# Performance work log

Hardware: AMD Instinct MI355X
Metric: run time of the kernel (lower is better)

## Reference

```python
import jax, jax.numpy as jnp
import numpy as np

LEAKY_SLOPE = 0.01  # torch nn.LeakyReLU default


def leaky_relu(x):
    return jnp.where(x >= 0, x, LEAKY_SLOPE * x)


def rgcn_conv(x, edge_index, edge_type, w_rel, w_root, b_conv):
    # PyG RGCNConv: out = x @ W_root + b + sum_r mean_{edges of rel r into i}(x_src @ W_r)
    n = x.shape[0]
    src, dst = edge_index[0], edge_index[1]
    out = x @ w_root + b_conv
    num_rel = w_rel.shape[0]
    for r in range(num_rel):  # small fixed relation count
        mask = (edge_type == r)
        msg = x[src] @ w_rel[r]                      # [E, H]
        msg = jnp.where(mask[:, None], msg, 0.0)
        agg = jax.ops.segment_sum(msg, dst, num_segments=n)          # [N, H]
        cnt = jax.ops.segment_sum(mask.astype(x.dtype), dst, num_segments=n)
        out = out + agg / jnp.maximum(cnt, 1.0)[:, None]             # mean aggr
    return out


def setup_inputs() -> dict:
    key = jax.random.key(0)
    ks = jax.random.split(key, 10)
    N, E, D_IN, H, OUT, R = 50000, 600000, 768, 128, 3, 2
    s_in = 1.0 / np.sqrt(D_IN)
    s_h = 1.0 / np.sqrt(H)
    return {
        "feature": jax.random.normal(ks[0], (N, D_IN), dtype=jnp.float32),
        "edge_index": jax.random.randint(ks[1], (2, E), 0, N, dtype=jnp.int64),
        "edge_type": jax.random.randint(ks[2], (E,), 0, R, dtype=jnp.int64),
        "w_in": jax.random.uniform(ks[3], (D_IN, H), jnp.float32, -s_in, s_in),
        "b_in": jax.random.uniform(ks[4], (H,), jnp.float32, -s_in, s_in),
        "w_rel": jax.random.uniform(ks[5], (R, H, H), jnp.float32, -s_h, s_h),
        "w_root": jax.random.uniform(ks[6], (H, H), jnp.float32, -s_h, s_h),
        "b_conv": jnp.zeros((H,), jnp.float32),
        "w_out": jax.random.uniform(ks[7], (H, OUT), jnp.float32, -s_h, s_h),
        "b_out": jax.random.uniform(ks[8], (OUT,), jnp.float32, -s_h, s_h),
    }


def reference(feature, edge_index, edge_type, w_in, b_in, w_rel, w_root, b_conv, w_out, b_out):
    x = leaky_relu(feature @ w_in + b_in)
    # NOTE: original forward applies rgcn1 twice (shared weights); dropout is
    # identity at inference; rgcn2/linear_relu_output1 are unused.
    x = rgcn_conv(x, edge_index, edge_type, w_rel, w_root, b_conv)
    x = rgcn_conv(x, edge_index, edge_type, w_rel, w_root, b_conv)
    return x @ w_out + b_out
```

## Files before the change

### kernel.cpp

```cpp
#include <hip/hip_runtime.h>

#define H 128
#define CAP 64

typedef _Float16 f16x8 __attribute__((ext_vector_type(8)));
typedef float    f32x4 __attribute__((ext_vector_type(4)));

__global__ __launch_bounds__(256) void hist_fill(const int* __restrict__ src,
    const int* __restrict__ dst, const int* __restrict__ et,
    int* __restrict__ cnt, int* __restrict__ elist, int E, int N)
{
    int e = blockIdx.x * 256 + threadIdx.x;
    if (e >= E) return;
    int s = src[e], d = dst[e], t = et[e];
    int b = t * N + d;
    int pos = atomicAdd(&cnt[b], 1);
    if (pos < CAP) elist[(size_t)b * CAP + pos] = s;
}

__global__ __launch_bounds__(256) void prep_w(const float* __restrict__ w_in,
    const float* __restrict__ w_root, const float* __restrict__ w_rel,
    _Float16* __restrict__ wInT, _Float16* __restrict__ wcatT, int K)
{
    int idx = blockIdx.x * 256 + threadIdx.x;
    int tot1 = K * H;
    if (idx < tot1) {
        int k = idx >> 7, c = idx & 127;
        int o = ((k >> 3) << 10) + (c << 3) + (k & 7);
        wInT[o] = (_Float16)w_in[idx];
    } else {
        int i2 = idx - tot1;
        if (i2 < H * 384) {
            int c = i2 / 384, k = i2 - c * 384;
            float v;
            if (k < 128)      v = w_root[(size_t)k * H + c];
            else if (k < 256) v = w_rel[(size_t)(k - 128) * H + c];
            else              v = w_rel[(size_t)H * H + (size_t)(k - 256) * H + c];
            wcatT[i2] = (_Float16)v;
        }
    }
}

__global__ __launch_bounds__(256) void prep_fin(const float* __restrict__ w_root,
    const float* __restrict__ w_rel, const float* __restrict__ b_conv,
    const float* __restrict__ w_out, const float* __restrict__ b_out,
    float* __restrict__ wfin, float* __restrict__ bfin, int OUT)
{
    int idx = blockIdx.x * 256 + threadIdx.x;
    int nw = 3 * H * OUT;
    if (idx < nw) {
        int mk = idx / OUT, c = idx - mk * OUT;
        int m = mk >> 7, k = mk & 127;
        const float* W = (m == 0) ? w_root : (w_rel + (size_t)(m - 1) * H * H);
        float s = 0.f;
        for (int j = 0; j < H; j++)
            s += W[(size_t)k * H + j] * w_out[(size_t)j * OUT + c];
        wfin[(size_t)mk * OUT + c] = s;
    } else if (idx < nw + OUT) {
        int c = idx - nw;
        float s = b_out[c];
        for (int j = 0; j < H; j++) s += b_conv[j] * w_out[(size_t)j * OUT + c];
        bfin[c] = s;
    }
}

__device__ __forceinline__ f16x8 cvt8(float4 v0, float4 v1) {
    f16x8 t;
    t[0] = (_Float16)v0.x; t[1] = (_Float16)v0.y; t[2] = (_Float16)v0.z; t[3] = (_Float16)v0.w;
    t[4] = (_Float16)v1.x; t[5] = (_Float16)v1.y; t[6] = (_Float16)v1.z; t[7] = (_Float16)v1.w;
    return t;
}

__global__ __launch_bounds__(256, 2) void gemm_big(const float* __restrict__ A,
    const _Float16* __restrict__ WP, const float* __restrict__ bias,
    _Float16* __restrict__ C16, int M, int K, int ldc)
{
    __shared__ float As[2][4][2048];

    const int tid = threadIdx.x;
    const int w   = tid >> 6;
    const int l   = tid & 63;
    const int l15 = l & 15;
    const int q   = l >> 4;
    const int brow = blockIdx.x * 64;
    const int wr   = w * 16;

    const int lh  = l >> 5;
    const int l31 = l & 31;

    const _Float16* bp = WP + ((size_t)q * H + l15) * 8;

    float bj[8];
#pragma unroll
    for (int j = 0; j < 8; j++) bj[j] = bias[j * 16 + l15];

    f32x4 acc[8];
    const f32x4 z4 = {0.f, 0.f, 0.f, 0.f};
#pragma unroll
    for (int j = 0; j < 8; j++) acc[j] = z4;

    const int chunks = K / 128;

#define STAGE(c, nbuf)                                                          \
    {                                                                           \
        _Pragma("unroll")                                                       \
        for (int i = 0; i < 8; i++) {                                           \
            int r  = 2 * i + lh;                                                \
            int gr = brow + wr + r; if (gr >= M) gr = M - 1;                    \
            int cg = l31 ^ (r & 7);                                             \
            const float* ga = A + (size_t)gr * K + (c) * 128 + cg * 4;          \
            __builtin_amdgcn_global_load_lds(                                   \
                (const __attribute__((address_space(1))) void*)ga,              \
                (__attribute__((address_space(3))) void*)&As[nbuf][w][i * 256], \
                16, 0, 0);                                                      \
        }                                                                       \
    }

    STAGE(0, 0);
    __syncthreads();

    for (int c = 0; c < chunks; c++) {
        if (c + 1 < chunks) STAGE(c + 1, (c + 1) & 1);

        const float* wbuf = As[c & 1][w];
#pragma unroll
        for (int ks = 0; ks < 4; ks++) {
            const int sl = ks * 4 + q;
            const int xr = l15 & 7;
            const int p0 = (2 * sl) ^ xr;
            const int p1 = (2 * sl + 1) ^ xr;
            float4 lo = *(const float4*)&wbuf[l15 * 128 + p0 * 4];
            float4 hi = *(const float4*)&wbuf[l15 * 128 + p1 * 4];
            f16x8 af = cvt8(lo, hi);
            const _Float16* bks = bp + (size_t)(c * 4 + ks) * 4096;
            f16x8 bf[8];
#pragma unroll
            for (int j = 0; j < 8; j++) bf[j] = *(const f16x8*)(bks + j * 128);
#pragma unroll
            for (int j = 0; j < 8; j++)
                acc[j] = __builtin_amdgcn_mfma_f32_16x16x32_f16(af, bf[j], acc[j], 0, 0, 0);
        }
        __syncthreads();
    }
#undef STAGE

#pragma unroll
    for (int rg = 0; rg < 4; rg++) {
        int row = brow + wr + q * 4 + rg;
        if (row < M) {
#pragma unroll
            for (int j = 0; j < 8; j++) {
                float v = acc[j][rg] + bj[j];
                v = (v >= 0.f) ? v : 0.01f * v;
                C16[(size_t)row * ldc + j * 16 + l15] = (_Float16)v;
            }
        }
    }
}

template<int MODE>
__global__ __launch_bounds__(256) void gather_k(const _Float16* __restrict__ X,
    int ldx, _Float16* __restrict__ Mout, const int* __restrict__ elist,
    const int* __restrict__ cnt, int N,
    const float* __restrict__ wfin, const float* __restrict__ bfin,
    float* __restrict__ out)
{
    int wv = blockIdx.x * 4 + (threadIdx.x >> 6);
    int l  = threadIdx.x & 63;
    if (wv >= N) return;

    const int eo   = l >> 4;
    const int e2   = eo & 1;
    const int half = l >> 5;
    const int c8   = (l & 15) * 8;

    int dr = cnt[(size_t)half * N + wv];
    int d  = dr < CAP ? dr : CAP;
    float inv = dr > 0 ? 1.f / (float)dr : 0.f;
    const int* lst = elist + ((size_t)half * N + wv) * CAP;

    float acc[8];
#pragma unroll
    for (int j = 0; j < 8; j++) acc[j] = 0.f;

    const f16x8 zv = {};
    for (int p = e2; p < d; p += 8) {
        int p1 = p + 2, p2 = p + 4, p3 = p + 6;
        int s0 = lst[p];
        f16x8 v0 = *(const f16x8*)&X[(size_t)s0 * ldx + c8];
        f16x8 v1 = zv, v2 = zv, v3 = zv;
        if (p1 < d) { int s = lst[p1]; v1 = *(const f16x8*)&X[(size_t)s * ldx + c8]; }
        if (p2 < d) { int s = lst[p2]; v2 = *(const f16x8*)&X[(size_t)s * ldx + c8]; }
        if (p3 < d) { int s = lst[p3]; v3 = *(const f16x8*)&X[(size_t)s * ldx + c8]; }
#pragma unroll
        for (int j = 0; j < 8; j++)
            acc[j] += (float)v0[j] + (float)v1[j] + (float)v2[j] + (float)v3[j];
    }

#pragma unroll
    for (int j = 0; j < 8; j++) {
        acc[j] += __shfl_xor(acc[j], 16);
        acc[j] *= inv;
    }

    if (MODE == 0) {
        if (eo == 0 || eo == 2) {
            f16x8 o;
#pragma unroll
            for (int j = 0; j < 8; j++) o[j] = (_Float16)acc[j];
            *(f16x8*)&Mout[(size_t)wv * 256 + half * 128 + c8] = o;
        }
    } else {
        float p0 = 0.f, p1 = 0.f, p2 = 0.f;
        if (eo == 1) {
            f16x8 xv = *(const f16x8*)&X[(size_t)wv * ldx + c8];
#pragma unroll
            for (int j = 0; j < 8; j++) {
                float xf = (float)xv[j];
                const float* wr = wfin + (size_t)(c8 + j) * 3;
                p0 += xf * wr[0]; p1 += xf * wr[1]; p2 += xf * wr[2];
            }
        } else if (eo == 0 || eo == 2) {
            const float* wb = wfin + (size_t)(eo == 0 ? 1 : 2) * H * 3;
#pragma unroll
            for (int j = 0; j < 8; j++) {
                const float* wr = wb + (size_t)(c8 + j) * 3;
                p0 += acc[j] * wr[0]; p1 += acc[j] * wr[1]; p2 += acc[j] * wr[2];
            }
        }
#pragma unroll
        for (int off = 1; off <= 32; off <<= 1) {
            p0 += __shfl_xor(p0, off);
            p1 += __shfl_xor(p1, off);
            p2 += __shfl_xor(p2, off);
        }
        if (l == 0) {
            out[(size_t)wv * 3 + 0] = p0 + bfin[0];
            out[(size_t)wv * 3 + 1] = p1 + bfin[1];
            out[(size_t)wv * 3 + 2] = p2 + bfin[2];
        }
    }
}

__global__ __launch_bounds__(512) void gemm_cat(const _Float16* __restrict__ X1,
    const _Float16* __restrict__ Mt, const _Float16* __restrict__ WT,
    const float* __restrict__ bias, _Float16* __restrict__ X2, int M, int mtiles)
{
    const int w   = threadIdx.x >> 6;
    const int l   = threadIdx.x & 63;
    const int l15 = l & 15;
    const int q   = l >> 4;
    const int col = w * 16 + l15;

    f16x8 bf[12];
    {
        const _Float16* wpp = WT + (size_t)col * 384 + q * 8;
#pragma unroll
        for (int c = 0; c < 12; c++) bf[c] = *(const f16x8*)(wpp + c * 32);
    }
    const float bj = bias[col];

    int t = blockIdx.x;
    if (t >= mtiles) return;
    f16x8 xf[12];
    {
        const _Float16* xp = X1 + ((size_t)t * 16 + l15) * 128 + q * 8;
        const _Float16* mp = Mt + ((size_t)t * 16 + l15) * 256 + q * 8;
#pragma unroll
        for (int c = 0; c < 4; c++) xf[c] = *(const f16x8*)(xp + c * 32);
#pragma unroll
        for (int c = 4; c < 12; c++) xf[c] = *(const f16x8*)(mp + (c - 4) * 32);
    }

    const f32x4 z4 = {0.f, 0.f, 0.f, 0.f};
    while (true) {
        int tn = t + gridDim.x;
        bool more = tn < mtiles;
        f16x8 xnf[12];
        if (more) {
            const _Float16* xp = X1 + ((size_t)tn * 16 + l15) * 128 + q * 8;
            const _Float16* mp = Mt + ((size_t)tn * 16 + l15) * 256 + q * 8;
#pragma unroll
            for (int c = 0; c < 4; c++) xnf[c] = *(const f16x8*)(xp + c * 32);
#pragma unroll
            for (int c = 4; c < 12; c++) xnf[c] = *(const f16x8*)(mp + (c - 4) * 32);
        }

        f32x4 a0 = z4;
#pragma unroll
        for (int c = 0; c < 12; c++)
            a0 = __builtin_amdgcn_mfma_f32_16x16x32_f16(xf[c], bf[c], a0, 0, 0, 0);

#pragma unroll
        for (int rg = 0; rg < 4; rg++) {
            int row = t * 16 + q * 4 + rg;
            if (row < M) X2[(size_t)row * 128 + col] = (_Float16)(a0[rg] + bj);
        }
        if (!more) break;
        t = tn;
#pragma unroll
        for (int c = 0; c < 12; c++) xf[c] = xnf[c];
    }
}

__global__ __launch_bounds__(256) void proj_generic(const _Float16* __restrict__ X2,
    const _Float16* __restrict__ Mt, const float* __restrict__ wfin,
    const float* __restrict__ bfin, float* __restrict__ out, int N, int OUT)
{
    int row = blockIdx.x * 4 + (threadIdx.x >> 6);
    int l = threadIdx.x & 63;
    if (row >= N) return;
    float xv[6];
#pragma unroll
    for (int i = 0; i < 6; i++) {
        int k = l * 6 + i;
        xv[i] = (k < 128) ? (float)X2[(size_t)row * 128 + k]
                          : (float)Mt[(size_t)row * 256 + (k - 128)];
    }
    for (int c = 0; c < OUT; c++) {
        float p = 0.f;
#pragma unroll
        for (int i = 0; i < 6; i++) p += xv[i] * wfin[(size_t)(l * 6 + i) * OUT + c];
        for (int off = 32; off > 0; off >>= 1) p += __shfl_down(p, off);
        if (l == 0) out[(size_t)row * OUT + c] = p + bfin[c];
    }
}

extern "C" void kernel_launch(void* const* d_in, const int* in_sizes, int n_in,
                              void* d_out, int out_size, void* d_ws, size_t ws_size,
                              hipStream_t stream) {
    const float* feature = (const float*)d_in[0];
    const int*   ei      = (const int*)d_in[1];
    const int*   et      = (const int*)d_in[2];
    const float* w_in    = (const float*)d_in[3];
    const float* b_in    = (const float*)d_in[4];
    const float* w_rel   = (const float*)d_in[5];
    const float* w_root  = (const float*)d_in[6];
    const float* b_conv  = (const float*)d_in[7];
    const float* w_out   = (const float*)d_in[8];
    const float* b_out   = (const float*)d_in[9];

    const int HH   = in_sizes[4];
    const int D_IN = in_sizes[3] / HH;
    const int N    = in_sizes[0] / D_IN;
    const int E    = in_sizes[1] / 2;
    const int OUT  = in_sizes[9];

    char* base = (char*)d_ws;
    _Float16* wInT  = (_Float16*)base;
    _Float16* wcatT = wInT + (size_t)D_IN * HH;
    _Float16* X1    = wcatT + (size_t)HH * 384;
    _Float16* X2    = X1 + (size_t)N * HH;
    _Float16* Mt    = X2 + (size_t)N * HH;
    float* wfin     = (float*)(Mt + (size_t)N * 256);
    float* bfin     = wfin + (size_t)3 * HH * (OUT > 0 ? OUT : 1);
    int* cnt        = (int*)(bfin + ((OUT + 3) & ~3));
    int* elist      = cnt + (size_t)2 * N;

    hipMemsetAsync(cnt, 0, sizeof(int) * (size_t)2 * N, stream);
    prep_w<<<(D_IN * HH + HH * 384 + 255) / 256, 256, 0, stream>>>(
        w_in, w_root, w_rel, wInT, wcatT, D_IN);
    prep_fin<<<(3 * HH * OUT + OUT + 255) / 256, 256, 0, stream>>>(
        w_root, w_rel, b_conv, w_out, b_out, wfin, bfin, OUT);
    hist_fill<<<(E + 255) / 256, 256, 0, stream>>>(ei, ei + E, et, cnt, elist, E, N);

    gemm_big<<<(N + 63) / 64, 256, 0, stream>>>(feature, wInT, b_in, X1, N, D_IN, HH);

    const int mtiles  = (N + 15) / 16;
    const int gblocks = (N + 3) / 4;

    gather_k<0><<<gblocks, 256, 0, stream>>>(X1, 128, Mt, elist, cnt, N,
                                             nullptr, nullptr, nullptr);
    gemm_cat<<<1024, 512, 0, stream>>>(X1, Mt, wcatT, b_conv, X2, N, mtiles);
    if (OUT == 3) {
        gather_k<1><<<gblocks, 256, 0, stream>>>(X2, 128, nullptr, elist, cnt, N,
                                                 wfin, bfin, (float*)d_out);
    } else {
        gather_k<0><<<gblocks, 256, 0, stream>>>(X2, 128, Mt, elist, cnt, N,
                                                 nullptr, nullptr, nullptr);
        proj_generic<<<gblocks, 256, 0, stream>>>(X2, Mt, wfin, bfin,
                                                  (float*)d_out, N, OUT);
    }
}
```

Baseline: 440.1 us.

## Fuse first-layer neighbor mean gather with concatenated root/relation GEMM

Adds a fused kernel that gathers per-relation neighbor means for 16 rows into shared memory, then immediately runs the [X | M0 | M1] x Wcat MFMA product and writes X2. This removes the intermediate Mt round-trip through global memory and one kernel launch on the OUT==3 path. The edge-list writes in hist_fill also become nontemporal stores. In exchange, each block reloads the full weight columns from global (no cross-tile reuse like gemm_cat), and gather parallelism per block is reduced.

```diff
diff --git a/kernel.cpp b/kernel.cpp
--- a/kernel.cpp
+++ b/kernel.cpp
@@ -15,7 +15,7 @@
     int s = src[e], d = dst[e], t = et[e];
     int b = t * N + d;
     int pos = atomicAdd(&cnt[b], 1);
-    if (pos < CAP) elist[(size_t)b * CAP + pos] = s;
+    if (pos < CAP) __builtin_nontemporal_store(s, &elist[(size_t)b * CAP + pos]);
 }
 
 __global__ __launch_bounds__(256) void prep_w(const float* __restrict__ w_in,
@@ -158,6 +158,96 @@
     }
 }
 
+__global__ __launch_bounds__(256) void fused_l1(const _Float16* __restrict__ X1,
+    const _Float16* __restrict__ WT, const float* __restrict__ bias,
+    const int* __restrict__ elist, const int* __restrict__ cnt,
+    _Float16* __restrict__ X2, int N)
+{
+    __shared__ _Float16 Ml[16][264];
+
+    const int w   = threadIdx.x >> 6;
+    const int l   = threadIdx.x & 63;
+    const int l15 = l & 15;
+    const int q   = l >> 4;
+    const int r0  = blockIdx.x * 16;
+
+    const int eo   = l >> 4;
+    const int e2   = eo & 1;
+    const int half = l >> 5;
+    const int c8   = l15 * 8;
+
+    const f16x8 zv = {};
+#pragma unroll
+    for (int i = 0; i < 4; i++) {
+        const int rl = w * 4 + i;
+        const int r  = r0 + rl;
+        float acc[8];
+#pragma unroll
+        for (int j = 0; j < 8; j++) acc[j] = 0.f;
+        float inv = 0.f;
+        if (r < N) {
+            int dr = cnt[(size_t)half * N + r];
+            int d  = dr < CAP ? dr : CAP;
+            inv = dr > 0 ? 1.f / (float)dr : 0.f;
+            const int* lst = elist + ((size_t)half * N + r) * CAP;
+            for (int p = e2; p < d; p += 8) {
+                int p1 = p + 2, p2 = p + 4, p3 = p + 6;
+                int s0 = lst[p];
+                f16x8 v0 = *(const f16x8*)&X1[(size_t)s0 * H + c8];
+                f16x8 v1 = zv, v2 = zv, v3 = zv;
+                if (p1 < d) { int s = lst[p1]; v1 = *(const f16x8*)&X1[(size_t)s * H + c8]; }
+                if (p2 < d) { int s = lst[p2]; v2 = *(const f16x8*)&X1[(size_t)s * H + c8]; }
+                if (p3 < d) { int s = lst[p3]; v3 = *(const f16x8*)&X1[(size_t)s * H + c8]; }
+#pragma unroll
+                for (int j = 0; j < 8; j++)
+                    acc[j] += (float)v0[j] + (float)v1[j] + (float)v2[j] + (float)v3[j];
+            }
+        }
+#pragma unroll
+        for (int j = 0; j < 8; j++) {
+            acc[j] += __shfl_xor(acc[j], 16);
+            acc[j] *= inv;
+        }
+        if (r < N && (eo == 0 || eo == 2)) {
+            f16x8 o;
+#pragma unroll
+            for (int j = 0; j < 8; j++) o[j] = (_Float16)acc[j];
+            *(f16x8*)&Ml[rl][half * 128 + c8] = o;
+        }
+    }
+    __syncthreads();
+
+    int gr = r0 + l15; if (gr >= N) gr = N - 1;
+    f16x8 xf[12];
+    {
+        const _Float16* xp = X1 + (size_t)gr * H + q * 8;
+#pragma unroll
+        for (int c = 0; c < 4; c++) xf[c] = *(const f16x8*)(xp + c * 32);
+#pragma unroll
+        for (int c = 4; c < 12; c++) xf[c] = *(const f16x8*)&Ml[l15][(c - 4) * 32 + q * 8];
+    }
+
+    const f32x4 z4 = {0.f, 0.f, 0.f, 0.f};
+#pragma unroll
+    for (int cf = 0; cf < 2; cf++) {
+        const int col = w * 32 + cf * 16 + l15;
+        f16x8 bf[12];
+        const _Float16* wpp = WT + (size_t)col * 384 + q * 8;
+#pragma unroll
+        for (int c = 0; c < 12; c++) bf[c] = *(const f16x8*)(wpp + c * 32);
+        f32x4 a0 = z4;
+#pragma unroll
+        for (int c = 0; c < 12; c++)
+            a0 = __builtin_amdgcn_mfma_f32_16x16x32_f16(xf[c], bf[c], a0, 0, 0, 0);
+        const float bj = bias[col];
+#pragma unroll
+        for (int rg = 0; rg < 4; rg++) {
+            int row = r0 + q * 4 + rg;
+            if (row < N) X2[(size_t)row * H + col] = (_Float16)(a0[rg] + bj);
+        }
+    }
+}
+
 template<int MODE>
 __global__ __launch_bounds__(256) void gather_k(const _Float16* __restrict__ X,
     int ldx, _Float16* __restrict__ Mout, const int* __restrict__ elist,
@@ -369,13 +459,14 @@
     const int mtiles  = (N + 15) / 16;
     const int gblocks = (N + 3) / 4;
 
-    gather_k<0><<<gblocks, 256, 0, stream>>>(X1, 128, Mt, elist, cnt, N,
-                                             nullptr, nullptr, nullptr);
-    gemm_cat<<<1024, 512, 0, stream>>>(X1, Mt, wcatT, b_conv, X2, N, mtiles);
     if (OUT == 3) {
+        fused_l1<<<mtiles, 256, 0, stream>>>(X1, wcatT, b_conv, elist, cnt, X2, N);
         gather_k<1><<<gblocks, 256, 0, stream>>>(X2, 128, nullptr, elist, cnt, N,
                                                  wfin, bfin, (float*)d_out);
     } else {
+        gather_k<0><<<gblocks, 256, 0, stream>>>(X1, 128, Mt, elist, cnt, N,
+                                                 nullptr, nullptr, nullptr);
+        gemm_cat<<<1024, 512, 0, stream>>>(X1, Mt, wcatT, b_conv, X2, N, mtiles);
         gather_k<0><<<gblocks, 256, 0, stream>>>(X2, 128, Mt, elist, cnt, N,
                                                  nullptr, nullptr, nullptr);
         proj_generic<<<gblocks, 256, 0, stream>>>(X2, Mt, wfin, bfin,
```

After: 421.1 us. 1.05x faster.
